# Performance work log

Hardware: AMD Instinct MI355X
Metric: run time of the kernel (lower is better)

Reference implementation:

```python
import jax, jax.numpy as jnp
import numpy as np

HIDDEN = 2048
N_HEADS = 16
HEAD_DIM = 128
N_KV_HEADS = 4
MAX_POS = 4096
NEG_INF = -1e9


def _fixed_pos_embedding(features, length):
    # matches generate_fixed_pos_embedding: freqs over arange(0, features, 2)/features
    fraction = jnp.arange(0, features, 2, dtype=jnp.float32) / features
    timescale = 10000.0 ** fraction
    inv_freq = 1.0 / timescale
    sinusoid = jnp.einsum('i,j->ij', jnp.arange(length, dtype=jnp.float32), inv_freq)
    sinusoid = jnp.concatenate([sinusoid, sinusoid], axis=-1)  # [length, features]
    return jnp.sin(sinusoid), jnp.cos(sinusoid)


def setup_inputs() -> dict:
    key = jax.random.key(0)
    k0, k1, k2, k3, k4 = jax.random.split(key, 5)
    B, S = 2, 2048
    hidden_states = jax.random.normal(k0, (B, S, HIDDEN), dtype=jnp.float32)
    # causal additive mask [B,1,S,S]; module forces mask[:, :, :, 0] = 0
    causal = jnp.where(jnp.tril(jnp.ones((S, S), dtype=bool)), 0.0, NEG_INF).astype(jnp.float32)
    causal = causal.at[:, 0].set(0.0)
    attention_mask = jnp.broadcast_to(causal[None, None], (B, 1, S, S))
    std = 0.02
    q_w = jax.random.normal(k1, (N_HEADS * HEAD_DIM, HIDDEN), dtype=jnp.float32) * std
    k_w = jax.random.normal(k2, (N_KV_HEADS * HEAD_DIM, HIDDEN), dtype=jnp.float32) * std
    v_w = jax.random.normal(k3, (N_KV_HEADS * HEAD_DIM, HIDDEN), dtype=jnp.float32) * std
    o_w = jax.random.normal(k4, (HIDDEN, N_HEADS * HEAD_DIM), dtype=jnp.float32) * std
    sin, cos = _fixed_pos_embedding(HEAD_DIM, MAX_POS)
    return {"hidden_states": hidden_states, "attention_mask": attention_mask,
            "q_w": q_w, "k_w": k_w, "v_w": v_w, "o_w": o_w, "sin": sin, "cos": cos}


def _rotate_half(x):
    d = x.shape[-1] // 2
    return jnp.concatenate([-x[..., d:], x[..., :d]], axis=-1)


def reference(hidden_states, attention_mask, q_w, k_w, v_w, o_w, sin, cos):
    B, S, _ = hidden_states.shape
    D = cos.shape[-1]
    H = q_w.shape[0] // D
    KV = k_w.shape[0] // D
    n_rep = H // KV

    # QKV projections (nn.Linear: y = x @ W^T), split into heads: [B,S,h,D]
    q = jnp.einsum('bsh,oh->bso', hidden_states, q_w).reshape(B, S, H, D)
    k = jnp.einsum('bsh,oh->bso', hidden_states, k_w).reshape(B, S, KV, D)
    v = jnp.einsum('bsh,oh->bso', hidden_states, v_w).reshape(B, S, KV, D)

    # rotary embedding (non-decode path: q and k share cos/sin[:S])
    c = cos[:S][None, :, None, :]
    s = sin[:S][None, :, None, :]
    q = q * c + _rotate_half(q) * s
    k = k * c + _rotate_half(k) * s

    # repeat_kv (repeat_interleave along head dim) for GQA
    k = jnp.repeat(k, n_rep, axis=2)  # [B,S,H,D]
    v = jnp.repeat(v, n_rep, axis=2)

    # NOTE: no 1/sqrt(D) scaling -- module uses softmax_scale=1.0
    scores = jnp.einsum('bqhd,bkhd->bhqk', q, k) + attention_mask
    weights = jax.nn.softmax(scores.astype(jnp.float32), axis=-1).astype(q.dtype)
    attn = jnp.einsum('bhqk,bkhd->bqhd', weights, v).reshape(B, S, H * D)
    return jnp.einsum('bso,ho->bsh', attn, o_w)
```

## Files before the change

kernel.cpp:

```cpp
#include <hip/hip_runtime.h>

typedef __bf16 bf16x8 __attribute__((ext_vector_type(8)));
typedef float f32x4 __attribute__((ext_vector_type(4)));

#define LOG2E 1.44269504088896340736f

#define GLDS16(g, l) __builtin_amdgcn_global_load_lds(                         \
    (const __attribute__((address_space(1))) unsigned int*)(g),                \
    (__attribute__((address_space(3))) unsigned int*)(l), 16, 0, 0)

__global__ __launch_bounds__(256) void split_matrix(
    const float* __restrict__ src, __bf16* __restrict__ dh, __bf16* __restrict__ dl)
{
    const size_t t = (size_t)(blockIdx.x * 256 + threadIdx.x) * 8;
    float4 a = *(const float4*)(src + t);
    float4 b = *(const float4*)(src + t + 4);
    float f[8] = {a.x, a.y, a.z, a.w, b.x, b.y, b.z, b.w};
    bf16x8 h, l;
#pragma unroll
    for (int i = 0; i < 8; ++i) {
        __bf16 hh = (__bf16)f[i];
        h[i] = hh; l[i] = (__bf16)(f[i] - (float)hh);
    }
    *(bf16x8*)(dh + t) = h;
    *(bf16x8*)(dl + t) = l;
}

__global__ __launch_bounds__(256) void gemm_planes(
    const __bf16* __restrict__ Ah, const __bf16* __restrict__ Al,
    const __bf16* __restrict__ Bh, const __bf16* __restrict__ Bl,
    float* __restrict__ C, int K, int ldc)
{
    __shared__ __bf16 sAh[128 * 32], sAl[128 * 32];
    __shared__ __bf16 sBh[128 * 32], sBl[128 * 32];

    const int tid  = threadIdx.x;
    const int lane = tid & 63;
    const int wave = tid >> 6;
    const int m0 = blockIdx.y * 128;
    const int n0 = blockIdx.x * 128;

    const int sr  = wave * 32 + (lane >> 2);
    const int sc  = (lane & 3) * 8;
    const __bf16* ga0 = Ah + (size_t)(m0 + sr) * K + sc;
    const __bf16* ga1 = ga0 + (size_t)16 * K;
    const __bf16* gA0 = Al + (size_t)(m0 + sr) * K + sc;
    const __bf16* gA1 = gA0 + (size_t)16 * K;
    const __bf16* gb0 = Bh + (size_t)(n0 + sr) * K + sc;
    const __bf16* gb1 = gb0 + (size_t)16 * K;
    const __bf16* gB0 = Bl + (size_t)(n0 + sr) * K + sc;
    const __bf16* gB1 = gB0 + (size_t)16 * K;
    __bf16* la0 = &sAh[(wave * 32) * 32];
    __bf16* la1 = &sAh[(wave * 32 + 16) * 32];
    __bf16* lA0 = &sAl[(wave * 32) * 32];
    __bf16* lA1 = &sAl[(wave * 32 + 16) * 32];
    __bf16* lb0 = &sBh[(wave * 32) * 32];
    __bf16* lb1 = &sBh[(wave * 32 + 16) * 32];
    __bf16* lB0 = &sBl[(wave * 32) * 32];
    __bf16* lB1 = &sBl[(wave * 32 + 16) * 32];

    f32x4 acc[4][4];
    for (int mi = 0; mi < 4; ++mi)
        for (int ni = 0; ni < 4; ++ni)
            acc[mi][ni] = (f32x4){0.f, 0.f, 0.f, 0.f};

    const int wm = (wave & 1) * 64;
    const int wn = (wave >> 1) * 64;
    const int fr = lane & 15;
    const int fc = (lane >> 4) * 8;
    const int dr = (lane >> 4) * 4;

    for (int k0 = 0; k0 < K; k0 += 32) {
        GLDS16(ga0, la0); GLDS16(ga1, la1);
        GLDS16(gA0, lA0); GLDS16(gA1, lA1);
        GLDS16(gb0, lb0); GLDS16(gb1, lb1);
        GLDS16(gB0, lB0); GLDS16(gB1, lB1);
        ga0 += 32; ga1 += 32; gA0 += 32; gA1 += 32;
        gb0 += 32; gb1 += 32; gB0 += 32; gB1 += 32;
        __syncthreads();

        bf16x8 afh[4], afl[4], bfh[4], bfl[4];
#pragma unroll
        for (int i = 0; i < 4; ++i) {
            afh[i] = *(const bf16x8*)&sAh[(wm + i * 16 + fr) * 32 + fc];
            afl[i] = *(const bf16x8*)&sAl[(wm + i * 16 + fr) * 32 + fc];
            bfh[i] = *(const bf16x8*)&sBh[(wn + i * 16 + fr) * 32 + fc];
            bfl[i] = *(const bf16x8*)&sBl[(wn + i * 16 + fr) * 32 + fc];
        }
#pragma unroll
        for (int mi = 0; mi < 4; ++mi)
#pragma unroll
            for (int ni = 0; ni < 4; ++ni) {
                acc[mi][ni] = __builtin_amdgcn_mfma_f32_16x16x32_bf16(
                    afh[mi], bfh[ni], acc[mi][ni], 0, 0, 0);
                acc[mi][ni] = __builtin_amdgcn_mfma_f32_16x16x32_bf16(
                    afl[mi], bfh[ni], acc[mi][ni], 0, 0, 0);
                acc[mi][ni] = __builtin_amdgcn_mfma_f32_16x16x32_bf16(
                    afh[mi], bfl[ni], acc[mi][ni], 0, 0, 0);
            }
        __syncthreads();
    }

    for (int mi = 0; mi < 4; ++mi)
        for (int ni = 0; ni < 4; ++ni)
            for (int r = 0; r < 4; ++r) {
                int row = m0 + wm + mi * 16 + dr + r;
                int col = n0 + wn + ni * 16 + fr;
                C[(size_t)row * ldc + col] = acc[mi][ni][r];
            }
}

__global__ __launch_bounds__(256) void rope_q(
    float* __restrict__ qkv,
    const float* __restrict__ sinp, const float* __restrict__ cosp)
{
    int t = blockIdx.x * 256 + threadIdx.x;
    int row = t >> 10;
    int rem = t & 1023;
    int col = (rem >> 6) * 128 + (rem & 63);
    int s = row & 2047;
    int d = col & 127;

    float* p = qkv + (size_t)row * 3072 + col;
    float x0  = p[0];
    float x1  = p[64];
    float c0  = cosp[s * 128 + d];
    float c1  = cosp[s * 128 + d + 64];
    float sn0 = sinp[s * 128 + d];
    float sn1 = sinp[s * 128 + d + 64];
    p[0]  = x0 * c0 - x1 * sn0;
    p[64] = x1 * c1 + x0 * sn1;
}

__global__ __launch_bounds__(256) void prep_kv(
    const float* __restrict__ qkv,
    const float* __restrict__ sinp, const float* __restrict__ cosp,
    __bf16* __restrict__ ksp, __bf16* __restrict__ vtsp)
{
    __shared__ float vs[32][132];

    const int tid = threadIdx.x;
    const int kb  = blockIdx.x;
    const int kvh = blockIdx.y;
    const int b   = blockIdx.z;

    {
        const int key = tid >> 1;
        const int dh  = (tid & 1) * 32;
        const int pos = kb * 128 + key;
        const float* src = qkv + (size_t)(b * 2048 + pos) * 3072 + 2048 + kvh * 128;
        __bf16* dst = ksp + ((size_t)((b * 4 + kvh) * 2048) + pos) * 256;
        const float* cp = cosp + pos * 128;
        const float* sp = sinp + pos * 128;
#pragma unroll
        for (int g = 0; g < 4; ++g) {
            int d0 = dh + g * 8;
            float4 x0a = *(const float4*)(src + d0);
            float4 x0b = *(const float4*)(src + d0 + 4);
            float4 x1a = *(const float4*)(src + d0 + 64);
            float4 x1b = *(const float4*)(src + d0 + 68);
            float4 c0a = *(const float4*)(cp + d0);
            float4 c0b = *(const float4*)(cp + d0 + 4);
            float4 c1a = *(const float4*)(cp + d0 + 64);
            float4 c1b = *(const float4*)(cp + d0 + 68);
            float4 s0a = *(const float4*)(sp + d0);
            float4 s0b = *(const float4*)(sp + d0 + 4);
            float4 s1a = *(const float4*)(sp + d0 + 64);
            float4 s1b = *(const float4*)(sp + d0 + 68);
            float x0[8] = {x0a.x,x0a.y,x0a.z,x0a.w,x0b.x,x0b.y,x0b.z,x0b.w};
            float x1[8] = {x1a.x,x1a.y,x1a.z,x1a.w,x1b.x,x1b.y,x1b.z,x1b.w};
            float c0[8] = {c0a.x,c0a.y,c0a.z,c0a.w,c0b.x,c0b.y,c0b.z,c0b.w};
            float c1[8] = {c1a.x,c1a.y,c1a.z,c1a.w,c1b.x,c1b.y,c1b.z,c1b.w};
            float s0[8] = {s0a.x,s0a.y,s0a.z,s0a.w,s0b.x,s0b.y,s0b.z,s0b.w};
            float s1[8] = {s1a.x,s1a.y,s1a.z,s1a.w,s1b.x,s1b.y,s1b.z,s1b.w};
            bf16x8 h0, l0, h1, l1;
#pragma unroll
            for (int i = 0; i < 8; ++i) {
                float y0 = x0[i] * c0[i] - x1[i] * s0[i];
                float y1 = x1[i] * c1[i] + x0[i] * s1[i];
                __bf16 hh0 = (__bf16)y0;
                __bf16 hh1 = (__bf16)y1;
                h0[i] = hh0; l0[i] = (__bf16)(y0 - (float)hh0);
                h1[i] = hh1; l1[i] = (__bf16)(y1 - (float)hh1);
            }
            *(bf16x8*)(dst + d0)            = h0;
            *(bf16x8*)(dst + d0 + 64)       = h1;
            *(bf16x8*)(dst + 128 + d0)      = l0;
            *(bf16x8*)(dst + 128 + d0 + 64) = l1;
        }
    }

    for (int st = 0; st < 4; ++st) {
        __syncthreads();
        {
            const int key = tid >> 3;
            const int dc  = (tid & 7) * 16;
            const float* vsrc = qkv + (size_t)(b * 2048 + kb * 128 + st * 32 + key) * 3072
                                + 2560 + kvh * 128 + dc;
            float4 v0 = *(const float4*)(vsrc);
            float4 v1 = *(const float4*)(vsrc + 4);
            float4 v2 = *(const float4*)(vsrc + 8);
            float4 v3 = *(const float4*)(vsrc + 12);
            *(float4*)&vs[key][dc]      = v0;
            *(float4*)&vs[key][dc + 4]  = v1;
            *(float4*)&vs[key][dc + 8]  = v2;
            *(float4*)&vs[key][dc + 12] = v3;
        }
        __syncthreads();
        {
            const int plane = tid >> 7;
            const int d     = tid & 127;
            bf16x8 ob[4];
#pragma unroll
            for (int k = 0; k < 32; ++k) {
                float x = vs[k][d];
                __bf16 hh = (__bf16)x;
                ob[k >> 3][k & 7] = plane ? (__bf16)(x - (float)hh) : hh;
            }
            __bf16* dst = vtsp + ((((size_t)(b * 4 + kvh) * 64 + kb * 4 + st) * 2 + plane)
                                  * 128 + d) * 32;
            *(bf16x8*)(dst)      = ob[0];
            *(bf16x8*)(dst + 8)  = ob[1];
            *(bf16x8*)(dst + 16) = ob[2];
            *(bf16x8*)(dst + 24) = ob[3];
        }
    }
}

__global__ __launch_bounds__(256, 2) void flash_attn(
    const float* __restrict__ qkv,
    const __bf16* __restrict__ ksp,
    const __bf16* __restrict__ vtsp,
    __bf16* __restrict__ attnh, __bf16* __restrict__ attnl)
{
    __shared__ __bf16 Ks[2][32][268];
    __shared__ __bf16 Vt[2][256][34];
    __shared__ float  Psf[4][16][33];

    const int tid  = threadIdx.x;
    const int lane = tid & 63;
    const int wave = tid >> 6;
    const int id   = blockIdx.x;
    const int pair = id & 7;
    const int kvh  = pair & 3;
    const int b    = pair >> 2;
    const int u    = id >> 3;
    const int qb   = (u >> 5) ? (u & 31) : 63 - (u & 31);
    const int h    = kvh * 4 + wave;

    const int fr = lane & 15;
    const int fc = (lane >> 4) * 8;
    const int dr = (lane >> 4) * 4;

    bf16x8 aqh[2][4], aql[2][4];
    for (int rs = 0; rs < 2; ++rs) {
        const size_t qrow = (size_t)(b * 2048 + qb * 32 + rs * 16 + fr) * 3072 + h * 128;
        for (int ks = 0; ks < 4; ++ks) {
            float4 qv[2];
            qv[0] = *(const float4*)(qkv + qrow + ks * 32 + fc);
            qv[1] = *(const float4*)(qkv + qrow + ks * 32 + fc + 4);
            const float* qf = (const float*)qv;
            bf16x8 h8, l8;
#pragma unroll
            for (int i = 0; i < 8; ++i) {
                float x = qf[i];
                __bf16 hh = (__bf16)x;
                h8[i] = hh; l8[i] = (__bf16)(x - (float)hh);
            }
            aqh[rs][ks] = h8; aql[rs][ks] = l8;
        }
    }

    bf16x8 ones;
#pragma unroll
    for (int i = 0; i < 8; ++i) ones[i] = (__bf16)1.0f;

    f32x4 o[2][8];
    for (int rs = 0; rs < 2; ++rs)
        for (int dg = 0; dg < 8; ++dg) o[rs][dg] = (f32x4){0.f, 0.f, 0.f, 0.f};
    f32x4 ls[2] = {(f32x4){0.f,0.f,0.f,0.f}, (f32x4){0.f,0.f,0.f,0.f}};

    const int ntiles = qb + 1;
    const __bf16* kbase = ksp + (size_t)(b * 4 + kvh) * 2048 * 256;
    const __bf16* vbase = vtsp + (size_t)(b * 4 + kvh) * 64 * 8192;

    const int kkey = tid >> 3;
    const int kchk = (tid & 7) * 32;

    for (int kt = 0; kt < ntiles; ++kt) {
        const int buf = kt & 1;
        const int k0 = kt * 32;
        {
            const __bf16* kg = kbase + (size_t)(k0 + kkey) * 256 + kchk;
            bf16x8 v0 = ((const bf16x8*)kg)[0];
            bf16x8 v1 = ((const bf16x8*)kg)[1];
            bf16x8 v2 = ((const bf16x8*)kg)[2];
            bf16x8 v3 = ((const bf16x8*)kg)[3];
            __bf16* d = &Ks[buf][kkey][kchk];
            ((bf16x8*)d)[0] = v0; ((bf16x8*)d)[1] = v1;
            ((bf16x8*)d)[2] = v2; ((bf16x8*)d)[3] = v3;
        }
        {
            const __bf16* vg = vbase + (size_t)kt * 8192 + tid * 32;
            bf16x8 v0 = ((const bf16x8*)vg)[0];
            bf16x8 v1 = ((const bf16x8*)vg)[1];
            bf16x8 v2 = ((const bf16x8*)vg)[2];
            bf16x8 v3 = ((const bf16x8*)vg)[3];
            __bf16* d = &Vt[buf][tid][0];
            ((bf16x8*)d)[0] = v0; ((bf16x8*)d)[1] = v1;
            ((bf16x8*)d)[2] = v2; ((bf16x8*)d)[3] = v3;
        }
        __syncthreads();

        f32x4 s[2][2];
        s[0][0] = s[0][1] = s[1][0] = s[1][1] = (f32x4){0.f, 0.f, 0.f, 0.f};
        for (int ks = 0; ks < 4; ++ks) {
            bf16x8 b0h = *(const bf16x8*)&Ks[buf][fr][ks * 32 + fc];
            bf16x8 b0l = *(const bf16x8*)&Ks[buf][fr][128 + ks * 32 + fc];
            bf16x8 b1h = *(const bf16x8*)&Ks[buf][16 + fr][ks * 32 + fc];
            bf16x8 b1l = *(const bf16x8*)&Ks[buf][16 + fr][128 + ks * 32 + fc];
            for (int rs = 0; rs < 2; ++rs) {
                s[rs][0] = __builtin_amdgcn_mfma_f32_16x16x32_bf16(aqh[rs][ks], b0h, s[rs][0], 0, 0, 0);
                s[rs][0] = __builtin_amdgcn_mfma_f32_16x16x32_bf16(aql[rs][ks], b0h, s[rs][0], 0, 0, 0);
                s[rs][0] = __builtin_amdgcn_mfma_f32_16x16x32_bf16(aqh[rs][ks], b0l, s[rs][0], 0, 0, 0);
                s[rs][1] = __builtin_amdgcn_mfma_f32_16x16x32_bf16(aqh[rs][ks], b1h, s[rs][1], 0, 0, 0);
                s[rs][1] = __builtin_amdgcn_mfma_f32_16x16x32_bf16(aql[rs][ks], b1h, s[rs][1], 0, 0, 0);
                s[rs][1] = __builtin_amdgcn_mfma_f32_16x16x32_bf16(aqh[rs][ks], b1l, s[rs][1], 0, 0, 0);
            }
        }

        bf16x8 ph[2], pl[2];
        for (int rs = 0; rs < 2; ++rs) {
            f32x4 s0 = s[rs][0], s1 = s[rs][1];
            for (int r = 0; r < 4; ++r) {
                int qg = qb * 32 + rs * 16 + dr + r;
                if (k0 + fr > qg)      s0[r] = -1e30f;
                if (k0 + 16 + fr > qg) s1[r] = -1e30f;
                s0[r] = exp2f(s0[r] * LOG2E);
                s1[r] = exp2f(s1[r] * LOG2E);
            }
            for (int r = 0; r < 4; ++r) {
                Psf[wave][dr + r][fr]      = s0[r];
                Psf[wave][dr + r][16 + fr] = s1[r];
            }
            asm volatile("s_waitcnt lgkmcnt(0)" ::: "memory");
            float4 pv[2];
            pv[0] = *(const float4*)&Psf[wave][fr][fc];
            pv[1] = *(const float4*)&Psf[wave][fr][fc + 4];
            asm volatile("s_waitcnt lgkmcnt(0)" ::: "memory");
            const float* pf = (const float*)pv;
#pragma unroll
            for (int i = 0; i < 8; ++i) {
                float x = pf[i];
                __bf16 hh = (__bf16)x;
                ph[rs][i] = hh; pl[rs][i] = (__bf16)(x - (float)hh);
            }
            ls[rs] = __builtin_amdgcn_mfma_f32_16x16x32_bf16(ph[rs], ones, ls[rs], 0, 0, 0);
            ls[rs] = __builtin_amdgcn_mfma_f32_16x16x32_bf16(pl[rs], ones, ls[rs], 0, 0, 0);
        }

        for (int dg = 0; dg < 8; ++dg) {
            bf16x8 bvh = *(const bf16x8*)&Vt[buf][dg * 16 + fr][fc];
            bf16x8 bvl = *(const bf16x8*)&Vt[buf][128 + dg * 16 + fr][fc];
            for (int rs = 0; rs < 2; ++rs) {
                o[rs][dg] = __builtin_amdgcn_mfma_f32_16x16x32_bf16(ph[rs], bvh, o[rs][dg], 0, 0, 0);
                o[rs][dg] = __builtin_amdgcn_mfma_f32_16x16x32_bf16(pl[rs], bvh, o[rs][dg], 0, 0, 0);
                o[rs][dg] = __builtin_amdgcn_mfma_f32_16x16x32_bf16(ph[rs], bvl, o[rs][dg], 0, 0, 0);
            }
        }
    }

    for (int rs = 0; rs < 2; ++rs) {
        const size_t orow = (size_t)(b * 2048 + qb * 32 + rs * 16);
        for (int dg = 0; dg < 8; ++dg)
            for (int r = 0; r < 4; ++r) {
                float val = o[rs][dg][r] / ls[rs][r];
                size_t idx = (orow + dr + r) * 2048 + h * 128 + dg * 16 + fr;
                __bf16 hh = (__bf16)val;
                attnh[idx] = hh;
                attnl[idx] = (__bf16)(val - (float)hh);
            }
    }
}

extern "C" void kernel_launch(void* const* d_in, const int* in_sizes, int n_in,
                              void* d_out, int out_size, void* d_ws, size_t ws_size,
                              hipStream_t stream)
{
    const float* hs   = (const float*)d_in[0];
    const float* qw   = (const float*)d_in[2];
    const float* kw   = (const float*)d_in[3];
    const float* vw   = (const float*)d_in[4];
    const float* ow   = (const float*)d_in[5];
    const float* sinp = (const float*)d_in[6];
    const float* cosp = (const float*)d_in[7];
    float* outp = (float*)d_out;

    char* w = (char*)d_ws;
    float*  qkv  = (float*)w;   w += (size_t)4096 * 3072 * 4;
    __bf16* ksp  = (__bf16*)w;  w += (size_t)8 * 2048 * 256 * 2;
    __bf16* vtsp = (__bf16*)w;  w += (size_t)8 * 64 * 8192 * 2;
    __bf16* wqh  = (__bf16*)w;  w += (size_t)3072 * 2048 * 2;
    __bf16* wql  = (__bf16*)w;  w += (size_t)3072 * 2048 * 2;
    __bf16* owh  = (__bf16*)w;  w += (size_t)2048 * 2048 * 2;
    __bf16* owl  = (__bf16*)w;  w += (size_t)2048 * 2048 * 2;
    __bf16* hsh  = (__bf16*)w;  w += (size_t)4096 * 2048 * 2;
    __bf16* hsl  = (__bf16*)w;  w += (size_t)4096 * 2048 * 2;
    __bf16* attnh = hsh;
    __bf16* attnl = hsl;

    split_matrix<<<4096, 256, 0, stream>>>(hs, hsh, hsl);
    split_matrix<<<2048, 256, 0, stream>>>(qw, wqh, wql);
    split_matrix<<<512,  256, 0, stream>>>(kw, wqh + (size_t)2048 * 2048,
                                               wql + (size_t)2048 * 2048);
    split_matrix<<<512,  256, 0, stream>>>(vw, wqh + (size_t)2560 * 2048,
                                               wql + (size_t)2560 * 2048);
    split_matrix<<<2048, 256, 0, stream>>>(ow, owh, owl);

    gemm_planes<<<dim3(24, 32), 256, 0, stream>>>(hsh, hsl, wqh, wql, qkv, 2048, 3072);
    rope_q<<<16384, 256, 0, stream>>>(qkv, sinp, cosp);
    prep_kv<<<dim3(16, 4, 2), 256, 0, stream>>>(qkv, sinp, cosp, ksp, vtsp);
    flash_attn<<<512, 256, 0, stream>>>(qkv, ksp, vtsp, attnh, attnl);
    gemm_planes<<<dim3(16, 32), 256, 0, stream>>>(attnh, attnl, owh, owl, outp, 2048, 2048);
}
```

Baseline: 603.1 us.

## Load K/V tiles via global_load_lds with XOR-swizzled layout, single buffer

The prep kernel now writes K and V^T in XOR-swizzled 16-byte chunks, so the attention kernel can copy tiles straight from global to LDS with global_load_lds. That drops the VGPR round trip and the padded arrays, and keeps LDS reads conflict-free through the matching swizzle. LDS drops to a single buffer, which lets occupancy rise to 3 blocks per CU. The change also adds s_setprio around the MFMA sections, applies causal masking only on the diagonal tile, and batches the P exchange for both row sets. In exchange, a single buffer means an extra barrier and no overlap of loads with compute.

```diff
diff --git a/kernel.cpp b/kernel.cpp
--- a/kernel.cpp
+++ b/kernel.cpp
@@ -148,6 +148,7 @@
         const int key = tid >> 1;
         const int dh  = (tid & 1) * 32;
         const int pos = kb * 128 + key;
+        const int ksw = key & 7;
         const float* src = qkv + (size_t)(b * 2048 + pos) * 3072 + 2048 + kvh * 128;
         __bf16* dst = ksp + ((size_t)((b * 4 + kvh) * 2048) + pos) * 256;
         const float* cp = cosp + pos * 128;
@@ -183,10 +184,11 @@
                 h0[i] = hh0; l0[i] = (__bf16)(y0 - (float)hh0);
                 h1[i] = hh1; l1[i] = (__bf16)(y1 - (float)hh1);
             }
-            *(bf16x8*)(dst + d0)            = h0;
-            *(bf16x8*)(dst + d0 + 64)       = h1;
-            *(bf16x8*)(dst + 128 + d0)      = l0;
-            *(bf16x8*)(dst + 128 + d0 + 64) = l1;
+            const int bb = d0 >> 3;
+            *(bf16x8*)(dst + ((bb        ^ ksw) << 3)) = h0;
+            *(bf16x8*)(dst + (((bb + 8)  ^ ksw) << 3)) = h1;
+            *(bf16x8*)(dst + (((bb + 16) ^ ksw) << 3)) = l0;
+            *(bf16x8*)(dst + (((bb + 24) ^ ksw) << 3)) = l1;
         }
     }
 
@@ -217,25 +219,27 @@
                 __bf16 hh = (__bf16)x;
                 ob[k >> 3][k & 7] = plane ? (__bf16)(x - (float)hh) : hh;
             }
-            __bf16* dst = vtsp + ((((size_t)(b * 4 + kvh) * 64 + kb * 4 + st) * 2 + plane)
-                                  * 128 + d) * 32;
-            *(bf16x8*)(dst)      = ob[0];
-            *(bf16x8*)(dst + 8)  = ob[1];
-            *(bf16x8*)(dst + 16) = ob[2];
-            *(bf16x8*)(dst + 24) = ob[3];
-        }
-    }
-}
-
-__global__ __launch_bounds__(256, 2) void flash_attn(
+            const int rV  = plane * 128 + d;
+            const int vsw = (d >> 1) & 3;
+            __bf16* dst = vtsp + ((size_t)((b * 4 + kvh) * 64 + kb * 4 + st)) * 8192
+                               + (size_t)rV * 32;
+            *(bf16x8*)(dst + ((0 ^ vsw) << 3)) = ob[0];
+            *(bf16x8*)(dst + ((1 ^ vsw) << 3)) = ob[1];
+            *(bf16x8*)(dst + ((2 ^ vsw) << 3)) = ob[2];
+            *(bf16x8*)(dst + ((3 ^ vsw) << 3)) = ob[3];
+        }
+    }
+}
+
+__global__ __launch_bounds__(256, 3) void flash_attn(
     const float* __restrict__ qkv,
     const __bf16* __restrict__ ksp,
     const __bf16* __restrict__ vtsp,
     __bf16* __restrict__ attnh, __bf16* __restrict__ attnl)
 {
-    __shared__ __bf16 Ks[2][32][268];
-    __shared__ __bf16 Vt[2][256][34];
-    __shared__ float  Psf[4][16][33];
+    __shared__ __bf16 Ks[32 * 256];
+    __shared__ __bf16 Vt[256 * 32];
+    __shared__ float  Psf[4][2][16][36];
 
     const int tid  = threadIdx.x;
     const int lane = tid & 63;
@@ -248,9 +252,11 @@
     const int qb   = (u >> 5) ? (u & 31) : 63 - (u & 31);
     const int h    = kvh * 4 + wave;
 
-    const int fr = lane & 15;
-    const int fc = (lane >> 4) * 8;
-    const int dr = (lane >> 4) * 4;
+    const int fr  = lane & 15;
+    const int g   = lane >> 4;
+    const int fc  = g * 8;
+    const int dr  = g * 4;
+    const int frs = fr & 7;
 
     bf16x8 aqh[2][4], aql[2][4];
     for (int rs = 0; rs < 2; ++rs) {
@@ -284,41 +290,37 @@
     const __bf16* kbase = ksp + (size_t)(b * 4 + kvh) * 2048 * 256;
     const __bf16* vbase = vtsp + (size_t)(b * 4 + kvh) * 64 * 8192;
 
-    const int kkey = tid >> 3;
-    const int kchk = (tid & 7) * 32;
-
     for (int kt = 0; kt < ntiles; ++kt) {
-        const int buf = kt & 1;
         const int k0 = kt * 32;
+
+        __syncthreads();
         {
-            const __bf16* kg = kbase + (size_t)(k0 + kkey) * 256 + kchk;
-            bf16x8 v0 = ((const bf16x8*)kg)[0];
-            bf16x8 v1 = ((const bf16x8*)kg)[1];
-            bf16x8 v2 = ((const bf16x8*)kg)[2];
-            bf16x8 v3 = ((const bf16x8*)kg)[3];
-            __bf16* d = &Ks[buf][kkey][kchk];
-            ((bf16x8*)d)[0] = v0; ((bf16x8*)d)[1] = v1;
-            ((bf16x8*)d)[2] = v2; ((bf16x8*)d)[3] = v3;
-        }
-        {
-            const __bf16* vg = vbase + (size_t)kt * 8192 + tid * 32;
-            bf16x8 v0 = ((const bf16x8*)vg)[0];
-            bf16x8 v1 = ((const bf16x8*)vg)[1];
-            bf16x8 v2 = ((const bf16x8*)vg)[2];
-            bf16x8 v3 = ((const bf16x8*)vg)[3];
-            __bf16* d = &Vt[buf][tid][0];
-            ((bf16x8*)d)[0] = v0; ((bf16x8*)d)[1] = v1;
-            ((bf16x8*)d)[2] = v2; ((bf16x8*)d)[3] = v3;
+            const __bf16* kg = kbase + (size_t)k0 * 256 + wave * 2048 + lane * 8;
+            const __bf16* vg = vbase + (size_t)kt * 8192 + wave * 2048 + lane * 8;
+            __bf16* kl = &Ks[wave * 2048];
+            __bf16* vl = &Vt[wave * 2048];
+            GLDS16(kg,        kl);
+            GLDS16(kg + 512,  kl + 512);
+            GLDS16(kg + 1024, kl + 1024);
+            GLDS16(kg + 1536, kl + 1536);
+            GLDS16(vg,        vl);
+            GLDS16(vg + 512,  vl + 512);
+            GLDS16(vg + 1024, vl + 1024);
+            GLDS16(vg + 1536, vl + 1536);
         }
         __syncthreads();
 
         f32x4 s[2][2];
         s[0][0] = s[0][1] = s[1][0] = s[1][1] = (f32x4){0.f, 0.f, 0.f, 0.f};
+        __builtin_amdgcn_s_setprio(1);
+#pragma unroll
         for (int ks = 0; ks < 4; ++ks) {
-            bf16x8 b0h = *(const bf16x8*)&Ks[buf][fr][ks * 32 + fc];
-            bf16x8 b0l = *(const bf16x8*)&Ks[buf][fr][128 + ks * 32 + fc];
-            bf16x8 b1h = *(const bf16x8*)&Ks[buf][16 + fr][ks * 32 + fc];
-            bf16x8 b1l = *(const bf16x8*)&Ks[buf][16 + fr][128 + ks * 32 + fc];
+            const int bh = ks * 4 + g;
+            bf16x8 b0h = *(const bf16x8*)&Ks[fr * 256        + ((bh        ^ frs) << 3)];
+            bf16x8 b0l = *(const bf16x8*)&Ks[fr * 256        + (((bh + 16) ^ frs) << 3)];
+            bf16x8 b1h = *(const bf16x8*)&Ks[(16 + fr) * 256 + ((bh        ^ frs) << 3)];
+            bf16x8 b1l = *(const bf16x8*)&Ks[(16 + fr) * 256 + (((bh + 16) ^ frs) << 3)];
+#pragma unroll
             for (int rs = 0; rs < 2; ++rs) {
                 s[rs][0] = __builtin_amdgcn_mfma_f32_16x16x32_bf16(aqh[rs][ks], b0h, s[rs][0], 0, 0, 0);
                 s[rs][0] = __builtin_amdgcn_mfma_f32_16x16x32_bf16(aql[rs][ks], b0h, s[rs][0], 0, 0, 0);
@@ -328,46 +330,70 @@
                 s[rs][1] = __builtin_amdgcn_mfma_f32_16x16x32_bf16(aqh[rs][ks], b1l, s[rs][1], 0, 0, 0);
             }
         }
-
-        bf16x8 ph[2], pl[2];
+        __builtin_amdgcn_s_setprio(0);
+
+        const bool diag = (kt == ntiles - 1);
+#pragma unroll
         for (int rs = 0; rs < 2; ++rs) {
             f32x4 s0 = s[rs][0], s1 = s[rs][1];
+            if (diag) {
+#pragma unroll
+                for (int r = 0; r < 4; ++r) {
+                    const int qg = qb * 32 + rs * 16 + dr + r;
+                    if (k0 + fr > qg)      s0[r] = -1e30f;
+                    if (k0 + 16 + fr > qg) s1[r] = -1e30f;
+                }
+            }
+#pragma unroll
             for (int r = 0; r < 4; ++r) {
-                int qg = qb * 32 + rs * 16 + dr + r;
-                if (k0 + fr > qg)      s0[r] = -1e30f;
-                if (k0 + 16 + fr > qg) s1[r] = -1e30f;
                 s0[r] = exp2f(s0[r] * LOG2E);
                 s1[r] = exp2f(s1[r] * LOG2E);
             }
+#pragma unroll
             for (int r = 0; r < 4; ++r) {
-                Psf[wave][dr + r][fr]      = s0[r];
-                Psf[wave][dr + r][16 + fr] = s1[r];
-            }
-            asm volatile("s_waitcnt lgkmcnt(0)" ::: "memory");
-            float4 pv[2];
-            pv[0] = *(const float4*)&Psf[wave][fr][fc];
-            pv[1] = *(const float4*)&Psf[wave][fr][fc + 4];
-            asm volatile("s_waitcnt lgkmcnt(0)" ::: "memory");
-            const float* pf = (const float*)pv;
+                Psf[wave][rs][dr + r][fr]      = s0[r];
+                Psf[wave][rs][dr + r][16 + fr] = s1[r];
+            }
+        }
+        asm volatile("s_waitcnt lgkmcnt(0)" ::: "memory");
+        float4 pva[2], pvb[2];
+        pva[0] = *(const float4*)&Psf[wave][0][fr][fc];
+        pva[1] = *(const float4*)&Psf[wave][0][fr][fc + 4];
+        pvb[0] = *(const float4*)&Psf[wave][1][fr][fc];
+        pvb[1] = *(const float4*)&Psf[wave][1][fr][fc + 4];
+        asm volatile("s_waitcnt lgkmcnt(0)" ::: "memory");
+        bf16x8 ph[2], pl[2];
+        {
+            const float* pf0 = (const float*)pva;
+            const float* pf1 = (const float*)pvb;
 #pragma unroll
             for (int i = 0; i < 8; ++i) {
-                float x = pf[i];
-                __bf16 hh = (__bf16)x;
-                ph[rs][i] = hh; pl[rs][i] = (__bf16)(x - (float)hh);
-            }
-            ls[rs] = __builtin_amdgcn_mfma_f32_16x16x32_bf16(ph[rs], ones, ls[rs], 0, 0, 0);
-            ls[rs] = __builtin_amdgcn_mfma_f32_16x16x32_bf16(pl[rs], ones, ls[rs], 0, 0, 0);
-        }
-
+                float x0 = pf0[i], x1 = pf1[i];
+                __bf16 h0 = (__bf16)x0, h1 = (__bf16)x1;
+                ph[0][i] = h0; pl[0][i] = (__bf16)(x0 - (float)h0);
+                ph[1][i] = h1; pl[1][i] = (__bf16)(x1 - (float)h1);
+            }
+        }
+
+        __builtin_amdgcn_s_setprio(1);
+        ls[0] = __builtin_amdgcn_mfma_f32_16x16x32_bf16(ph[0], ones, ls[0], 0, 0, 0);
+        ls[0] = __builtin_amdgcn_mfma_f32_16x16x32_bf16(pl[0], ones, ls[0], 0, 0, 0);
+        ls[1] = __builtin_amdgcn_mfma_f32_16x16x32_bf16(ph[1], ones, ls[1], 0, 0, 0);
+        ls[1] = __builtin_amdgcn_mfma_f32_16x16x32_bf16(pl[1], ones, ls[1], 0, 0, 0);
+#pragma unroll
         for (int dg = 0; dg < 8; ++dg) {
-            bf16x8 bvh = *(const bf16x8*)&Vt[buf][dg * 16 + fr][fc];
-            bf16x8 bvl = *(const bf16x8*)&Vt[buf][128 + dg * 16 + fr][fc];
+            const int d0 = dg * 16 + fr;
+            const int sw = (g ^ ((d0 >> 1) & 3)) << 3;
+            bf16x8 bvh = *(const bf16x8*)&Vt[d0 * 32 + sw];
+            bf16x8 bvl = *(const bf16x8*)&Vt[(d0 + 128) * 32 + sw];
+#pragma unroll
             for (int rs = 0; rs < 2; ++rs) {
                 o[rs][dg] = __builtin_amdgcn_mfma_f32_16x16x32_bf16(ph[rs], bvh, o[rs][dg], 0, 0, 0);
                 o[rs][dg] = __builtin_amdgcn_mfma_f32_16x16x32_bf16(pl[rs], bvh, o[rs][dg], 0, 0, 0);
                 o[rs][dg] = __builtin_amdgcn_mfma_f32_16x16x32_bf16(ph[rs], bvl, o[rs][dg], 0, 0, 0);
             }
         }
+        __builtin_amdgcn_s_setprio(0);
     }
 
     for (int rs = 0; rs < 2; ++rs) {
```

Result: no change. 611.7 us (+1.4%).
